# Kernel tuning notes

Hardware: AMD Instinct MI355X
Metric: run time of the kernel (lower is better)

Reference implementation:

```python
import jax, jax.numpy as jnp
import numpy as np

N_NODES = 50000

def _lgconv(x, src, dst, norm):
    # gather-scale-scatter: out[i] = sum_{(j->i)} norm_e * x[j]
    msgs = x[src] * norm[:, None]                      # [E, d]
    return jax.ops.segment_sum(msgs, dst, num_segments=N_NODES)  # [N, d]

def setup_inputs() -> dict:
    key = jax.random.key(0)
    k1, k2 = jax.random.split(key)
    x = jax.random.normal(k1, (N_NODES, 128), dtype=jnp.float32)
    edge_index = jax.random.randint(k2, (2, 600000), 0, N_NODES, dtype=jnp.int64)
    return {"x": x, "edge_index": edge_index}

def reference(x, edge_index):
    src, dst = edge_index[0], edge_index[1]
    # PyG gcn_norm (no self loops, edge_weight = 1):
    deg = jax.ops.segment_sum(jnp.ones_like(src, dtype=x.dtype), dst, num_segments=N_NODES)
    dinv = jnp.where(deg > 0, jax.lax.rsqrt(jnp.where(deg > 0, deg, 1.0)), 0.0)
    norm = dinv[src] * dinv[dst]                       # [E]
    # Three stacked LGConv + relu (dropout is identity in eval mode)
    x = jax.nn.relu(_lgconv(x, src, dst, norm))
    x = jax.nn.relu(_lgconv(x, src, dst, norm))
    x = jax.nn.relu(_lgconv(x, src, dst, norm))
    return x
```

## Files before the change

### kernel.cpp

```cpp
#include <hip/hip_runtime.h>
#include <hip/hip_fp16.h>

#define NN 50000
#define FEAT 128
#define CSTRIDE 16

__global__ void init_kernel(const unsigned int* ei32, int* flag, int* hist, int n) {
    int i = blockIdx.x * 256 + threadIdx.x;
    if (i < n) hist[i] = 0;
    if (blockIdx.x == 0) {
        __shared__ int ok;
        if (threadIdx.x == 0) ok = 1;
        __syncthreads();
        if (ei32[2 * threadIdx.x + 1] != 0u) ok = 0;
        __syncthreads();
        if (threadIdx.x == 0) *flag = ok;
    }
}

static __device__ __forceinline__ void load_edge(const void* ei, int is64, int E, int e,
                                                 int& src, int& dst) {
    if (is64) {
        const long long* p = (const long long*)ei;
        src = (int)p[e];
        dst = (int)p[E + e];
    } else {
        const int* p = (const int*)ei;
        src = p[e];
        dst = p[E + e];
    }
}

__global__ void hist_kernel(const void* ei, const int* flag, int* hist, int E) {
    int base = (blockIdx.x * blockDim.x + threadIdx.x) * 4;
    if (base >= E) return;
    const int is64 = *flag;
    int n = E - base; if (n > 4) n = 4;
    int src[4], dst[4];
    #pragma unroll
    for (int i = 0; i < 4; ++i)
        if (i < n) load_edge(ei, is64, E, base + i, src[i], dst[i]);
    #pragma unroll
    for (int i = 0; i < 4; ++i)
        if (i < n) atomicAdd(&hist[dst[i]], 1);
}

__global__ void scan_local_kernel(const int* __restrict__ hist, int* __restrict__ local_excl,
                                  int* __restrict__ bsum, float* __restrict__ dinv, int n) {
    __shared__ int sdata[256];
    int i = blockIdx.x * 256 + threadIdx.x;
    int v = (i < n) ? hist[i] : 0;
    if (i < n) dinv[i] = (v > 0) ? rsqrtf((float)v) : 0.0f;
    sdata[threadIdx.x] = v;
    __syncthreads();
    for (int d = 1; d < 256; d <<= 1) {
        int t = (threadIdx.x >= (unsigned)d) ? sdata[threadIdx.x - d] : 0;
        __syncthreads();
        sdata[threadIdx.x] += t;
        __syncthreads();
    }
    if (i < n) local_excl[i] = sdata[threadIdx.x] - v;
    if (threadIdx.x == 255) bsum[blockIdx.x] = sdata[255];
}

__global__ void scan_bsum_kernel(int* bsum, int nb) {
    __shared__ int sdata[1024];
    int v = ((int)threadIdx.x < nb) ? bsum[threadIdx.x] : 0;
    sdata[threadIdx.x] = v;
    __syncthreads();
    for (int d = 1; d < 1024; d <<= 1) {
        int t = (threadIdx.x >= (unsigned)d) ? sdata[threadIdx.x - d] : 0;
        __syncthreads();
        sdata[threadIdx.x] += t;
        __syncthreads();
    }
    if ((int)threadIdx.x < nb) bsum[threadIdx.x] = sdata[threadIdx.x] - v;
}

__global__ void scan_add_kernel(const int* __restrict__ local_excl, const int* __restrict__ bsum,
                                int* __restrict__ rowp, int* __restrict__ curs, int n, int E) {
    int i = blockIdx.x * 256 + threadIdx.x;
    if (i < n) {
        int r = local_excl[i] + bsum[i >> 8];
        rowp[i] = r;
        curs[i * CSTRIDE] = r;
    }
    if (i == 0) rowp[n] = E;
}

__global__ void scatter_kernel(const void* ei, const int* flag, int* cursor,
                               unsigned long long* __restrict__ edge,
                               const float* __restrict__ dinv, int E) {
    int base = (blockIdx.x * blockDim.x + threadIdx.x) * 4;
    if (base >= E) return;
    const int is64 = *flag;
    int n = E - base; if (n > 4) n = 4;

    int src[4], dst[4];
    #pragma unroll
    for (int i = 0; i < 4; ++i)
        if (i < n) load_edge(ei, is64, E, base + i, src[i], dst[i]);

    float ds[4], dd[4];
    #pragma unroll
    for (int i = 0; i < 4; ++i)
        if (i < n) { ds[i] = dinv[src[i]]; dd[i] = dinv[dst[i]]; }

    int pos[4];
    #pragma unroll
    for (int i = 0; i < 4; ++i)
        if (i < n) pos[i] = atomicAdd(&cursor[dst[i] * CSTRIDE], 1);

    #pragma unroll
    for (int i = 0; i < 4; ++i)
        if (i < n) {
            float w = ds[i] * dd[i];
            edge[pos[i]] = (unsigned long long)(unsigned int)src[i] |
                           ((unsigned long long)(unsigned int)__float_as_int(w) << 32);
        }
}

static __device__ __forceinline__ float4 relu4(float4 v) {
    v.x = fmaxf(v.x, 0.0f); v.y = fmaxf(v.y, 0.0f);
    v.z = fmaxf(v.z, 0.0f); v.w = fmaxf(v.w, 0.0f);
    return v;
}

static __device__ __forceinline__ void fma4(float4& a, float w, float4 v) {
    a.x += w * v.x; a.y += w * v.y; a.z += w * v.z; a.w += w * v.w;
}

static __device__ __forceinline__ float4 h4_to_f4(uint2 r) {
    __half2 lo = *reinterpret_cast<__half2*>(&r.x);
    __half2 hi = *reinterpret_cast<__half2*>(&r.y);
    float2 f0 = __half22float2(lo);
    float2 f1 = __half22float2(hi);
    return make_float4(f0.x, f0.y, f1.x, f1.y);
}

static __device__ __forceinline__ uint2 f4_to_h4(float4 v) {
    __half2 lo = __floats2half2_rn(v.x, v.y);
    __half2 hi = __floats2half2_rn(v.z, v.w);
    uint2 r;
    r.x = *reinterpret_cast<unsigned int*>(&lo);
    r.y = *reinterpret_cast<unsigned int*>(&hi);
    return r;
}

__global__ void cvt_f2h_kernel(const float4* __restrict__ in, uint2* __restrict__ outh, int n4) {
    int i = blockIdx.x * blockDim.x + threadIdx.x;
    if (i >= n4) return;
    outh[i] = f4_to_h4(in[i]);
}

template <bool OUT_HALF>
__global__ void conv_h_kernel(const uint2* __restrict__ xh,
                              const int* __restrict__ row_ptr,
                              const unsigned long long* __restrict__ edge,
                              void* __restrict__ outbuf) {
    int gid = blockIdx.x * blockDim.x + threadIdx.x;
    int node = gid >> 5;
    int f4   = gid & 31;
    if (node >= NN) return;
    int beg = row_ptr[node];
    int end = row_ptr[node + 1];

    float4 a0 = make_float4(0.f, 0.f, 0.f, 0.f);
    float4 a1 = a0, a2 = a0, a3 = a0;

    for (int cb = beg; cb < end; cb += 32) {
        int rem = end - cb;
        if (rem > 32) rem = 32;
        int myi = (f4 < rem) ? f4 : 0;
        unsigned long long pk = edge[cb + myi];

        for (int j = 0; j < rem; j += 8) {
            int i0 = j + 0, i1 = j + 1, i2 = j + 2, i3 = j + 3;
            int i4 = j + 4, i5 = j + 5, i6 = j + 6, i7 = j + 7;
            int last = rem - 1;
            unsigned long long l0 = __shfl(pk, i0 < rem ? i0 : last, 32);
            unsigned long long l1 = __shfl(pk, i1 < rem ? i1 : last, 32);
            unsigned long long l2 = __shfl(pk, i2 < rem ? i2 : last, 32);
            unsigned long long l3 = __shfl(pk, i3 < rem ? i3 : last, 32);
            unsigned long long l4 = __shfl(pk, i4 < rem ? i4 : last, 32);
            unsigned long long l5 = __shfl(pk, i5 < rem ? i5 : last, 32);
            unsigned long long l6 = __shfl(pk, i6 < rem ? i6 : last, 32);
            unsigned long long l7 = __shfl(pk, i7 < rem ? i7 : last, 32);

            float w0 = (i0 < rem) ? __int_as_float((int)(l0 >> 32)) : 0.0f;
            float w1 = (i1 < rem) ? __int_as_float((int)(l1 >> 32)) : 0.0f;
            float w2 = (i2 < rem) ? __int_as_float((int)(l2 >> 32)) : 0.0f;
            float w3 = (i3 < rem) ? __int_as_float((int)(l3 >> 32)) : 0.0f;
            float w4 = (i4 < rem) ? __int_as_float((int)(l4 >> 32)) : 0.0f;
            float w5 = (i5 < rem) ? __int_as_float((int)(l5 >> 32)) : 0.0f;
            float w6 = (i6 < rem) ? __int_as_float((int)(l6 >> 32)) : 0.0f;
            float w7 = (i7 < rem) ? __int_as_float((int)(l7 >> 32)) : 0.0f;

            uint2 r0 = xh[(int)(unsigned int)l0 * 32 + f4];
            uint2 r1 = xh[(int)(unsigned int)l1 * 32 + f4];
            uint2 r2 = xh[(int)(unsigned int)l2 * 32 + f4];
            uint2 r3 = xh[(int)(unsigned int)l3 * 32 + f4];
            uint2 r4 = xh[(int)(unsigned int)l4 * 32 + f4];
            uint2 r5 = xh[(int)(unsigned int)l5 * 32 + f4];
            uint2 r6 = xh[(int)(unsigned int)l6 * 32 + f4];
            uint2 r7 = xh[(int)(unsigned int)l7 * 32 + f4];

            fma4(a0, w0, h4_to_f4(r0));
            fma4(a1, w1, h4_to_f4(r1));
            fma4(a2, w2, h4_to_f4(r2));
            fma4(a3, w3, h4_to_f4(r3));
            fma4(a0, w4, h4_to_f4(r4));
            fma4(a1, w5, h4_to_f4(r5));
            fma4(a2, w6, h4_to_f4(r6));
            fma4(a3, w7, h4_to_f4(r7));
        }
    }

    float4 acc;
    acc.x = (a0.x + a1.x) + (a2.x + a3.x);
    acc.y = (a0.y + a1.y) + (a2.y + a3.y);
    acc.z = (a0.z + a1.z) + (a2.z + a3.z);
    acc.w = (a0.w + a1.w) + (a2.w + a3.w);
    acc = relu4(acc);

    if (OUT_HALF) {
        ((uint2*)outbuf)[node * 32 + f4] = f4_to_h4(acc);
    } else {
        ((float4*)outbuf)[node * 32 + f4] = acc;
    }
}

__global__ void deg_kernel(const void* ei, const int* flag, float* deg, int E) {
    int e = blockIdx.x * blockDim.x + threadIdx.x;
    if (e >= E) return;
    int src, dst;
    load_edge(ei, *flag, E, e, src, dst);
    atomicAdd(&deg[dst], 1.0f);
}

__global__ void dinv_kernel(float* deg) {
    int i = blockIdx.x * blockDim.x + threadIdx.x;
    if (i >= NN) return;
    float d = deg[i];
    deg[i] = (d > 0.0f) ? (1.0f / sqrtf(d)) : 0.0f;
}

template <bool RELU_IN>
__global__ void conv_atomic_kernel(const float* __restrict__ xin, const void* ei, const int* flag,
                                   const float* __restrict__ dinv, float* __restrict__ yout, int E) {
    int gid = blockIdx.x * blockDim.x + threadIdx.x;
    int e  = gid >> 5;
    int f4 = gid & 31;
    if (e >= E) return;
    int src, dst;
    load_edge(ei, *flag, E, e, src, dst);
    float w = dinv[src] * dinv[dst];
    float4 v = ((const float4*)xin)[src * 32 + f4];
    if (RELU_IN) v = relu4(v);
    float* o = yout + (size_t)dst * FEAT + f4 * 4;
    atomicAdd(o + 0, v.x * w);
    atomicAdd(o + 1, v.y * w);
    atomicAdd(o + 2, v.z * w);
    atomicAdd(o + 3, v.w * w);
}

__global__ void relu_kernel(float4* buf, int n4) {
    int i = blockIdx.x * blockDim.x + threadIdx.x;
    if (i >= n4) return;
    buf[i] = relu4(buf[i]);
}

extern "C" void kernel_launch(void* const* d_in, const int* in_sizes, int n_in,
                              void* d_out, int out_size, void* d_ws, size_t ws_size,
                              hipStream_t stream) {
    const float* x  = (const float*)d_in[0];
    const void*  ei = d_in[1];
    const int E = in_sizes[1] / 2;

    float* out = (float*)d_out;
    char*  ws  = (char*)d_ws;

    const size_t feat_bytes  = (size_t)NN * FEAT * sizeof(float);
    const size_t half_bytes  = (size_t)NN * FEAT * sizeof(unsigned short);
    const int NB = (NN + 255) / 256;
    const int N4 = NN * 32;

    const size_t OFF_FLAG = 0;
    const size_t OFF_HIST = 1024;
    const size_t OFF_DINV = OFF_HIST + (((size_t)NN * 4 + 255) & ~255ull);
    const size_t OFF_ROWP = OFF_DINV + (((size_t)NN * 4 + 255) & ~255ull);
    const size_t OFF_CURS = OFF_ROWP + ((((size_t)NN + 1) * 4 + 255) & ~255ull);
    const size_t OFF_BSUM = OFF_CURS + (((size_t)NN * 4 * CSTRIDE + 255) & ~255ull);
    const size_t OFF_EDG  = OFF_BSUM + ((1024 * 4 + 255) & ~255ull);
    const size_t OFF_HA   = OFF_EDG + (((size_t)E * 8 + 255) & ~255ull);
    const size_t OFF_HB   = OFF_HA + ((half_bytes + 255) & ~255ull);
    const size_t NEEDED   = OFF_HB + half_bytes;

    int* flag = (int*)(ws + OFF_FLAG);

    if (ws_size >= NEEDED) {
        int*   hist = (int*)(ws + OFF_HIST);
        float* dinv = (float*)(ws + OFF_DINV);
        int*   rowp = (int*)(ws + OFF_ROWP);
        int*   curs = (int*)(ws + OFF_CURS);
        int*   bsum = (int*)(ws + OFF_BSUM);
        unsigned long long* edge = (unsigned long long*)(ws + OFF_EDG);
        uint2* hA   = (uint2*)(ws + OFF_HA);
        uint2* hB   = (uint2*)(ws + OFF_HB);

        init_kernel<<<NB, 256, 0, stream>>>((const unsigned int*)ei, flag, hist, NN);

        const int e4_blocks = (E / 4 + 255) / 256 + 1;
        hist_kernel<<<e4_blocks, 256, 0, stream>>>(ei, flag, hist, E);
        scan_local_kernel<<<NB, 256, 0, stream>>>(hist, rowp, bsum, dinv, NN);
        scan_bsum_kernel<<<1, 1024, 0, stream>>>(bsum, NB);
        scan_add_kernel<<<NB, 256, 0, stream>>>(rowp, bsum, rowp, curs, NN, E);
        scatter_kernel<<<e4_blocks, 256, 0, stream>>>(ei, flag, curs, edge, dinv, E);

        cvt_f2h_kernel<<<(N4 + 255) / 256, 256, 0, stream>>>((const float4*)x, hA, N4);

        const int conv_blocks = (NN * 32 + 255) / 256;
        conv_h_kernel<true><<<conv_blocks, 256, 0, stream>>>(hA, rowp, edge, hB);
        conv_h_kernel<true><<<conv_blocks, 256, 0, stream>>>(hB, rowp, edge, hA);
        conv_h_kernel<false><<<conv_blocks, 256, 0, stream>>>(hA, rowp, edge, out);
    } else {
        float* dinv = (float*)(ws + 1024);
        float* y    = (float*)(ws + 262144);

        hipMemsetAsync(dinv, 0, NN * sizeof(float), stream);
        hipMemsetAsync(out, 0, feat_bytes, stream);
        hipMemsetAsync(y, 0, feat_bytes, stream);

        init_kernel<<<1, 256, 0, stream>>>((const unsigned int*)ei, flag, (int*)(ws + 512), 256);
        deg_kernel<<<(E + 255) / 256, 256, 0, stream>>>(ei, flag, dinv, E);
        dinv_kernel<<<(NN + 255) / 256, 256, 0, stream>>>(dinv);

        const int conv_blocks = (int)(((size_t)E * 32 + 255) / 256);
        conv_atomic_kernel<false><<<conv_blocks, 256, 0, stream>>>(x, ei, flag, dinv, out, E);
        conv_atomic_kernel<true><<<conv_blocks, 256, 0, stream>>>(out, ei, flag, dinv, y, E);
        hipMemsetAsync(out, 0, feat_bytes, stream);
        conv_atomic_kernel<true><<<conv_blocks, 256, 0, stream>>>(y, ei, flag, dinv, out, E);
        relu_kernel<<<(out_size / 4 + 255) / 256, 256, 0, stream>>>((float4*)out, out_size / 4);
    }
}
```

Baseline: 153.4 us.

## Factor edge norm into per-node dinv scaling and store int32 column indices

Drops the per-edge weight dinv[src]*dinv[dst]. The source factor is applied to the features up front (inside the fp16 conversion, and after relu when a layer writes half output), and the destination factor is applied once per node after aggregation. The edge array shrinks from 8-byte packed (src, weight) pairs to 4-byte column indices, which halves CSR index traffic in every conv pass and removes the dinv gathers from the scatter kernel. The conversion kernel is launched earlier, right after dinv is computed. Folding the source scale into the fp16 features changes rounding slightly.

```diff
diff --git a/kernel.cpp b/kernel.cpp
--- a/kernel.cpp
+++ b/kernel.cpp
@@ -89,8 +89,7 @@
 }
 
 __global__ void scatter_kernel(const void* ei, const int* flag, int* cursor,
-                               unsigned long long* __restrict__ edge,
-                               const float* __restrict__ dinv, int E) {
+                               int* __restrict__ col, int E) {
     int base = (blockIdx.x * blockDim.x + threadIdx.x) * 4;
     if (base >= E) return;
     const int is64 = *flag;
@@ -101,11 +100,6 @@
     for (int i = 0; i < 4; ++i)
         if (i < n) load_edge(ei, is64, E, base + i, src[i], dst[i]);
 
-    float ds[4], dd[4];
-    #pragma unroll
-    for (int i = 0; i < 4; ++i)
-        if (i < n) { ds[i] = dinv[src[i]]; dd[i] = dinv[dst[i]]; }
-
     int pos[4];
     #pragma unroll
     for (int i = 0; i < 4; ++i)
@@ -113,11 +107,7 @@
 
     #pragma unroll
     for (int i = 0; i < 4; ++i)
-        if (i < n) {
-            float w = ds[i] * dd[i];
-            edge[pos[i]] = (unsigned long long)(unsigned int)src[i] |
-                           ((unsigned long long)(unsigned int)__float_as_int(w) << 32);
-        }
+        if (i < n) col[pos[i]] = src[i];
 }
 
 static __device__ __forceinline__ float4 relu4(float4 v) {
@@ -147,16 +137,21 @@
     return r;
 }
 
-__global__ void cvt_f2h_kernel(const float4* __restrict__ in, uint2* __restrict__ outh, int n4) {
+__global__ void cvt_f2h_kernel(const float4* __restrict__ in, const float* __restrict__ dinv,
+                               uint2* __restrict__ outh, int n4) {
     int i = blockIdx.x * blockDim.x + threadIdx.x;
     if (i >= n4) return;
-    outh[i] = f4_to_h4(in[i]);
+    float dd = dinv[i >> 5];
+    float4 v = in[i];
+    v.x *= dd; v.y *= dd; v.z *= dd; v.w *= dd;
+    outh[i] = f4_to_h4(v);
 }
 
 template <bool OUT_HALF>
 __global__ void conv_h_kernel(const uint2* __restrict__ xh,
                               const int* __restrict__ row_ptr,
-                              const unsigned long long* __restrict__ edge,
+                              const int* __restrict__ col,
+                              const float* __restrict__ dinv,
                               void* __restrict__ outbuf) {
     int gid = blockIdx.x * blockDim.x + threadIdx.x;
     int node = gid >> 5;
@@ -164,6 +159,7 @@
     if (node >= NN) return;
     int beg = row_ptr[node];
     int end = row_ptr[node + 1];
+    float dd = dinv[node];
 
     float4 a0 = make_float4(0.f, 0.f, 0.f, 0.f);
     float4 a1 = a0, a2 = a0, a3 = a0;
@@ -172,38 +168,38 @@
         int rem = end - cb;
         if (rem > 32) rem = 32;
         int myi = (f4 < rem) ? f4 : 0;
-        unsigned long long pk = edge[cb + myi];
+        int pk = col[cb + myi];
 
         for (int j = 0; j < rem; j += 8) {
             int i0 = j + 0, i1 = j + 1, i2 = j + 2, i3 = j + 3;
             int i4 = j + 4, i5 = j + 5, i6 = j + 6, i7 = j + 7;
             int last = rem - 1;
-            unsigned long long l0 = __shfl(pk, i0 < rem ? i0 : last, 32);
-            unsigned long long l1 = __shfl(pk, i1 < rem ? i1 : last, 32);
-            unsigned long long l2 = __shfl(pk, i2 < rem ? i2 : last, 32);
-            unsigned long long l3 = __shfl(pk, i3 < rem ? i3 : last, 32);
-            unsigned long long l4 = __shfl(pk, i4 < rem ? i4 : last, 32);
-            unsigned long long l5 = __shfl(pk, i5 < rem ? i5 : last, 32);
-            unsigned long long l6 = __shfl(pk, i6 < rem ? i6 : last, 32);
-            unsigned long long l7 = __shfl(pk, i7 < rem ? i7 : last, 32);
-
-            float w0 = (i0 < rem) ? __int_as_float((int)(l0 >> 32)) : 0.0f;
-            float w1 = (i1 < rem) ? __int_as_float((int)(l1 >> 32)) : 0.0f;
-            float w2 = (i2 < rem) ? __int_as_float((int)(l2 >> 32)) : 0.0f;
-            float w3 = (i3 < rem) ? __int_as_float((int)(l3 >> 32)) : 0.0f;
-            float w4 = (i4 < rem) ? __int_as_float((int)(l4 >> 32)) : 0.0f;
-            float w5 = (i5 < rem) ? __int_as_float((int)(l5 >> 32)) : 0.0f;
-            float w6 = (i6 < rem) ? __int_as_float((int)(l6 >> 32)) : 0.0f;
-            float w7 = (i7 < rem) ? __int_as_float((int)(l7 >> 32)) : 0.0f;
-
-            uint2 r0 = xh[(int)(unsigned int)l0 * 32 + f4];
-            uint2 r1 = xh[(int)(unsigned int)l1 * 32 + f4];
-            uint2 r2 = xh[(int)(unsigned int)l2 * 32 + f4];
-            uint2 r3 = xh[(int)(unsigned int)l3 * 32 + f4];
-            uint2 r4 = xh[(int)(unsigned int)l4 * 32 + f4];
-            uint2 r5 = xh[(int)(unsigned int)l5 * 32 + f4];
-            uint2 r6 = xh[(int)(unsigned int)l6 * 32 + f4];
-            uint2 r7 = xh[(int)(unsigned int)l7 * 32 + f4];
+            int c0 = __shfl(pk, i0 < rem ? i0 : last, 32);
+            int c1 = __shfl(pk, i1 < rem ? i1 : last, 32);
+            int c2 = __shfl(pk, i2 < rem ? i2 : last, 32);
+            int c3 = __shfl(pk, i3 < rem ? i3 : last, 32);
+            int c4 = __shfl(pk, i4 < rem ? i4 : last, 32);
+            int c5 = __shfl(pk, i5 < rem ? i5 : last, 32);
+            int c6 = __shfl(pk, i6 < rem ? i6 : last, 32);
+            int c7 = __shfl(pk, i7 < rem ? i7 : last, 32);
+
+            float w0 = (i0 < rem) ? 1.0f : 0.0f;
+            float w1 = (i1 < rem) ? 1.0f : 0.0f;
+            float w2 = (i2 < rem) ? 1.0f : 0.0f;
+            float w3 = (i3 < rem) ? 1.0f : 0.0f;
+            float w4 = (i4 < rem) ? 1.0f : 0.0f;
+            float w5 = (i5 < rem) ? 1.0f : 0.0f;
+            float w6 = (i6 < rem) ? 1.0f : 0.0f;
+            float w7 = (i7 < rem) ? 1.0f : 0.0f;
+
+            uint2 r0 = xh[c0 * 32 + f4];
+            uint2 r1 = xh[c1 * 32 + f4];
+            uint2 r2 = xh[c2 * 32 + f4];
+            uint2 r3 = xh[c3 * 32 + f4];
+            uint2 r4 = xh[c4 * 32 + f4];
+            uint2 r5 = xh[c5 * 32 + f4];
+            uint2 r6 = xh[c6 * 32 + f4];
+            uint2 r7 = xh[c7 * 32 + f4];
 
             fma4(a0, w0, h4_to_f4(r0));
             fma4(a1, w1, h4_to_f4(r1));
@@ -221,9 +217,11 @@
     acc.y = (a0.y + a1.y) + (a2.y + a3.y);
     acc.z = (a0.z + a1.z) + (a2.z + a3.z);
     acc.w = (a0.w + a1.w) + (a2.w + a3.w);
+    acc.x *= dd; acc.y *= dd; acc.z *= dd; acc.w *= dd;
     acc = relu4(acc);
 
     if (OUT_HALF) {
+        acc.x *= dd; acc.y *= dd; acc.z *= dd; acc.w *= dd;
         ((uint2*)outbuf)[node * 32 + f4] = f4_to_h4(acc);
     } else {
         ((float4*)outbuf)[node * 32 + f4] = acc;
@@ -292,7 +290,7 @@
     const size_t OFF_CURS = OFF_ROWP + ((((size_t)NN + 1) * 4 + 255) & ~255ull);
     const size_t OFF_BSUM = OFF_CURS + (((size_t)NN * 4 * CSTRIDE + 255) & ~255ull);
     const size_t OFF_EDG  = OFF_BSUM + ((1024 * 4 + 255) & ~255ull);
-    const size_t OFF_HA   = OFF_EDG + (((size_t)E * 8 + 255) & ~255ull);
+    const size_t OFF_HA   = OFF_EDG + (((size_t)E * 4 + 255) & ~255ull);
     const size_t OFF_HB   = OFF_HA + ((half_bytes + 255) & ~255ull);
     const size_t NEEDED   = OFF_HB + half_bytes;
 
@@ -304,7 +302,7 @@
         int*   rowp = (int*)(ws + OFF_ROWP);
         int*   curs = (int*)(ws + OFF_CURS);
         int*   bsum = (int*)(ws + OFF_BSUM);
-        unsigned long long* edge = (unsigned long long*)(ws + OFF_EDG);
+        int*   col  = (int*)(ws + OFF_EDG);
         uint2* hA   = (uint2*)(ws + OFF_HA);
         uint2* hB   = (uint2*)(ws + OFF_HB);
 
@@ -313,16 +311,15 @@
         const int e4_blocks = (E / 4 + 255) / 256 + 1;
         hist_kernel<<<e4_blocks, 256, 0, stream>>>(ei, flag, hist, E);
         scan_local_kernel<<<NB, 256, 0, stream>>>(hist, rowp, bsum, dinv, NN);
+        cvt_f2h_kernel<<<(N4 + 255) / 256, 256, 0, stream>>>((const float4*)x, dinv, hA, N4);
         scan_bsum_kernel<<<1, 1024, 0, stream>>>(bsum, NB);
         scan_add_kernel<<<NB, 256, 0, stream>>>(rowp, bsum, rowp, curs, NN, E);
-        scatter_kernel<<<e4_blocks, 256, 0, stream>>>(ei, flag, curs, edge, dinv, E);
-
-        cvt_f2h_kernel<<<(N4 + 255) / 256, 256, 0, stream>>>((const float4*)x, hA, N4);
+        scatter_kernel<<<e4_blocks, 256, 0, stream>>>(ei, flag, curs, col, E);
 
         const int conv_blocks = (NN * 32 + 255) / 256;
-        conv_h_kernel<true><<<conv_blocks, 256, 0, stream>>>(hA, rowp, edge, hB);
-        conv_h_kernel<true><<<conv_blocks, 256, 0, stream>>>(hB, rowp, edge, hA);
-        conv_h_kernel<false><<<conv_blocks, 256, 0, stream>>>(hA, rowp, edge, out);
+        conv_h_kernel<true><<<conv_blocks, 256, 0, stream>>>(hA, rowp, col, dinv, hB);
+        conv_h_kernel<true><<<conv_blocks, 256, 0, stream>>>(hB, rowp, col, dinv, hA);
+        conv_h_kernel<false><<<conv_blocks, 256, 0, stream>>>(hA, rowp, col, dinv, out);
     } else {
         float* dinv = (float*)(ws + 1024);
         float* y    = (float*)(ws + 262144);
```

Result: faster. 149.5 us (-2.5%).
